# Kernel optimization log

Hardware: AMD Instinct MI355X
Metric: run time of the kernel (lower is better)

The kernel has to match this reference:

```python
import jax, jax.numpy as jnp
import numpy as np

N = 768                       # atoms
E = N * (N - 1)               # complete directed graph edges
DIM = 64                      # hidden dim
CUT = 5.0                     # rbf high
NC = 50                       # n_centers = ceil(5/0.1)
ODIM = 1                      # output_dim
NCONV = 3
_centers_np = np.linspace(0.0, CUT, NC)
CENTERS = jnp.asarray(_centers_np, jnp.float32)
GAP = float(_centers_np[1] - _centers_np[0])
RO_IN = 2 * ODIM + NC         # readout input: 2*output_dim + rbf fan_out = 52


def softplus_bt(x, beta, thr):
    # torch.nn.Softplus(beta, threshold): linear above threshold
    bx = beta * x
    return jnp.where(bx > thr, x, jax.nn.softplus(bx) / beta)


def rbf(d):
    # exp(-(1/gap) * (d - mu_k)^2); d: (..., 1) -> (..., NC)
    return jnp.exp((-1.0 / GAP) * (d - CENTERS) ** 2)


def setup_inputs() -> dict:
    key = jax.random.key(0)
    ks = jax.random.split(key, 24)
    atom_types = jax.random.randint(ks[0], (N,), 0, 100)
    edge_distances = jax.random.uniform(ks[1], (E, 1), jnp.float32) * CUT
    # complete directed graph, edge order matches the nested i,j loop (i!=j)
    ii = np.repeat(np.arange(N), N)
    jj = np.tile(np.arange(N), N)
    m = ii != jj
    src = jnp.asarray(ii[m], jnp.int32)
    dst = jnp.asarray(jj[m], jnp.int32)

    def p(k, shape, fan):
        return jax.random.normal(k, shape, jnp.float32) / np.sqrt(fan)

    embedding = p(ks[2], (100, DIM), DIM).at[0].set(0.0)  # padding_idx=0
    L = NCONV
    return {
        'atom_types': atom_types, 'edge_distances': edge_distances,
        'src': src, 'dst': dst, 'embedding': embedding,
        'w1': p(ks[3], (L, DIM, DIM), DIM),                 # node_layer1 (no bias)
        'pw1': p(ks[4], (L, NC, DIM), NC), 'pb1': p(ks[5], (L, DIM), NC),
        'pw2': p(ks[6], (L, DIM, DIM), DIM), 'pb2': p(ks[7], (L, DIM), DIM),
        'qw1': p(ks[8], (L, DIM, DIM), DIM), 'qb1': p(ks[9], (L, DIM), DIM),
        'qw2': p(ks[10], (L, DIM, DIM), DIM), 'qb2': p(ks[11], (L, DIM), DIM),
        'au_w1': p(ks[12], (DIM, 64), DIM), 'au_b1': p(ks[13], (64,), DIM),
        'au_w2': p(ks[14], (64, ODIM), 64), 'au_b2': p(ks[15], (ODIM,), 64),
        'ro_w1': p(ks[16], (RO_IN, 64), RO_IN), 'ro_b1': p(ks[17], (64,), RO_IN),
        'ro_w2': p(ks[18], (64, 2), 64), 'ro_b2': p(ks[19], (2,), 64),
    }


def reference(atom_types, edge_distances, src, dst, embedding,
              w1, pw1, pb1, pw2, pb2, qw1, qb1, qw2, qb2,
              au_w1, au_b1, au_w2, au_b2, ro_w1, ro_b1, ro_w2, ro_b2):
    h = embedding[atom_types]                       # (N, DIM)
    rbf_out = rbf(edge_distances)                   # (E, NC)
    for l in range(NCONV):
        nw = h @ w1[l]                              # node weights (N, DIM)
        e = softplus_bt(rbf_out @ pw1[l] + pb1[l], 0.5, 14) @ pw2[l] + pb2[l]  # (E, DIM)
        msg = nw[src] * e                           # gather-mul (E, DIM)
        agg = jax.ops.segment_sum(msg, dst, num_segments=N)  # scatter-sum (N, DIM)
        upd = softplus_bt(agg @ qw1[l] + qb1[l], 0.5, 14) @ qw2[l] + qb2[l]
        h = h + upd
    # atom_update with ShiftSoftplus (beta=1, shift=2, threshold=20)
    ha = softplus_bt(h @ au_w1 + au_b1, 1.0, 20) - jnp.log(jnp.float32(2.0))
    ha = ha @ au_w2 + au_b2                         # (N, ODIM)
    # readout over all ordered pairs i!=j, in edge order == (src, dst)
    edge_feat = jnp.concatenate([ha[src], ha[dst], rbf_out], axis=-1)  # (E, 52)
    logits = jax.nn.relu(edge_feat @ ro_w1 + ro_b1) @ ro_w2 + ro_b2    # (E, 2)
    return jax.nn.softmax(logits, axis=-1)
```

## Files before the change

kernel.cpp:

```cpp
#include <hip/hip_runtime.h>

#define NATOMS 768
#define NM1    767
#define NEDGE  (768*767)
#define DIM    64
#define NC     50
#define GAPF   (5.0f/49.0f)
#define NIGAP  (-49.0f/5.0f)
#define G      512
#define STEPF  (5.0f/511.0f)
#define INVSTEP (511.0f/5.0f)
#define LN2F   0.693147180559945f

#define WS_H     0
#define WS_NWA   49152
#define WS_NWB   98304
#define WS_HA    147456
#define WS_DISTT 148224
#define WS_TT    738048

__device__ __forceinline__ float softplus05(float x) {
    float bx = 0.5f * x;
    return (bx > 14.0f) ? x : 2.0f * __logf(1.0f + __expf(bx));
}
__device__ __forceinline__ int lane_bcast_i(int v, int l) {
    return __builtin_amdgcn_readlane(v, l);
}
__device__ __forceinline__ float lane_bcast_f(float v, int l) {
    return __uint_as_float((unsigned)__builtin_amdgcn_readlane((int)__float_as_uint(v), l));
}

__global__ __launch_bounds__(256)
void k_pre(const int* __restrict__ types, const float* __restrict__ dist,
           const float* __restrict__ emb, const float* __restrict__ w1all,
           const float* __restrict__ pw1, const float* __restrict__ pb1,
           const float* __restrict__ pw2, const float* __restrict__ pb2,
           const float* __restrict__ row1, const float* __restrict__ rob1,
           float* __restrict__ ws) {
    __shared__ float s_t[4 * 64];
    const int tid = threadIdx.x, widx = tid >> 6, c = tid & 63;
    float* h     = ws + WS_H;
    float* nw    = ws + WS_NWA;
    float* distT = ws + WS_DISTT;
    float* TTf   = ws + WS_TT;
    const int b = blockIdx.x;

    if (b < 512) {
        const int w = b * 4 + widx, tbl = w >> 9, g = w & 511;
        const float d = g * STEPF;
        float val;
        if (tbl < 3) {
            const float* W1 = pw1 + tbl * NC * DIM;
            float t1 = pb1[tbl * DIM + c];
            for (int k = 0; k < NC; ++k) {
                float x = d - GAPF * (float)k;
                t1 = fmaf(__expf(NIGAP * x * x), W1[k * DIM + c], t1);
            }
            s_t[widx * 64 + c] = softplus05(t1);
            const float* W2 = pw2 + tbl * DIM * DIM;
            val = pb2[tbl * DIM + c];
            #pragma unroll 8
            for (int k = 0; k < DIM; ++k)
                val = fmaf(s_t[widx * 64 + k], W2[k * DIM + c], val);
        } else {
            val = rob1[c];
            for (int k = 0; k < NC; ++k) {
                float x = d - GAPF * (float)k;
                val = fmaf(__expf(NIGAP * x * x), row1[(2 + k) * DIM + c], val);
            }
        }
        float* TTt = TTf + tbl * (G * DIM * 2);
        TTt[(g * DIM + c) * 2] = val;
        if (g > 0) TTt[((g - 1) * DIM + c) * 2 + 1] = val;
    } else if (b < 704) {
        const int i = (b - 512) * 4 + widx;
        float hv = emb[types[i] * DIM + c];
        h[i * DIM + c] = hv;
        s_t[widx * 64 + c] = hv;
        float acc = 0.0f;
        #pragma unroll 8
        for (int k = 0; k < DIM; ++k)
            acc = fmaf(s_t[widx * 64 + k], w1all[k * DIM + c], acc);
        nw[i * DIM + c] = acc;
    } else {
        const int idx = (b - 704) * 256 + tid;
        const int j = idx / NATOMS, i = idx - j * NATOMS;
        distT[idx] = (i == j) ? 0.0f : dist[i * NM1 + (j - (j > i))];
    }
}

__global__ __launch_bounds__(512)
void k_edgeupd(const float2* __restrict__ TTl, const float* __restrict__ distT,
               const float* __restrict__ nwin,
               const float* __restrict__ qw1, const float* __restrict__ qb1,
               const float* __restrict__ qw2, const float* __restrict__ qb2,
               float* __restrict__ h,
               const float* __restrict__ wnext, float* __restrict__ nwout,
               const float* __restrict__ auw1, const float* __restrict__ aub1,
               const float* __restrict__ auw2, const float* __restrict__ aub2,
               float* __restrict__ ha, int last) {
    __shared__ float s_part[8][64];
    __shared__ float s_upd[192];
    const int tid = threadIdx.x, widx = tid >> 6, c = tid & 63;
    const int j = blockIdx.x;
    const int s0 = widx * 96;

    const char* TTb = (const char*)TTl + c * 8;
    float csum = 0.0f;
    {
        float d = distT[j * NATOMS + s0 + c];
        float pos = d * INVSTEP;
        int g = (int)pos;
        g = (g < 0) ? 0 : ((g > 510) ? 510 : g);
        float f = pos - (float)g;
        int kx = g * 512;
        #pragma unroll 8
        for (int it = 0; it < 64; ++it) {
            int kxu = lane_bcast_i(kx, it);
            float fu = lane_bcast_f(f, it);
            float2 tt = *(const float2*)(TTb + kxu);
            float e = fmaf(fu, tt.y - tt.x, tt.x);
            csum = fmaf(e, nwin[(s0 + it) * DIM + c], csum);
        }
    }
    {
        float d = distT[j * NATOMS + s0 + 64 + (c & 31)];
        float pos = d * INVSTEP;
        int g = (int)pos;
        g = (g < 0) ? 0 : ((g > 510) ? 510 : g);
        float f = pos - (float)g;
        int kx = g * 512;
        #pragma unroll 8
        for (int it = 0; it < 32; ++it) {
            int kxu = lane_bcast_i(kx, it);
            float fu = lane_bcast_f(f, it);
            float2 tt = *(const float2*)(TTb + kxu);
            float e = fmaf(fu, tt.y - tt.x, tt.x);
            csum = fmaf(e, nwin[(s0 + 64 + it) * DIM + c], csum);
        }
    }
    s_part[widx][c] = csum;
    __syncthreads();

    if (widx == 0) {
        float tot = 0.0f;
        #pragma unroll
        for (int w8 = 0; w8 < 8; ++w8) tot += s_part[w8][c];
        float2 t0 = *(const float2*)TTb;
        tot -= t0.x * nwin[j * DIM + c];
        s_upd[c] = tot;
        float t = qb1[c];
        #pragma unroll 8
        for (int k = 0; k < DIM; ++k) t = fmaf(s_upd[k], qw1[k * DIM + c], t);
        s_upd[64 + c] = softplus05(t);
        float o = qb2[c];
        #pragma unroll 8
        for (int k = 0; k < DIM; ++k) o = fmaf(s_upd[64 + k], qw2[k * DIM + c], o);
        float hn = h[j * DIM + c] + o;
        h[j * DIM + c] = hn;
        s_upd[128 + c] = hn;
        if (!last) {
            float v = 0.0f;
            #pragma unroll 8
            for (int k = 0; k < DIM; ++k) v = fmaf(s_upd[128 + k], wnext[k * DIM + c], v);
            nwout[j * DIM + c] = v;
        } else {
            float t2 = aub1[c];
            #pragma unroll 8
            for (int k = 0; k < DIM; ++k) t2 = fmaf(s_upd[128 + k], auw1[k * DIM + c], t2);
            t2 = ((t2 > 20.0f) ? t2 : __logf(1.0f + __expf(t2))) - LN2F;
            float v = t2 * auw2[c];
            #pragma unroll
            for (int s = 32; s > 0; s >>= 1) v += __shfl_down(v, s, 64);
            if (c == 0) ha[j] = v + aub2[0];
        }
    }
}

__global__ __launch_bounds__(256)
void k_ro(const float* __restrict__ dist, const int* __restrict__ src,
          const int* __restrict__ dst, const float* __restrict__ ha,
          const float2* __restrict__ TTro,
          const float* __restrict__ row1, const float* __restrict__ row2,
          const float* __restrict__ rob2, float* __restrict__ out) {
    __shared__ float4 s_pre[4][64];
    __shared__ float s_h[4][16 * 65];
    __shared__ float s_w2[128];
    const int tid = threadIdx.x, widx = tid >> 6, c = tid & 63;
    if (tid < 128) s_w2[tid] = row2[tid];
    __syncthreads();
    const int ebase = (blockIdx.x * 4 + widx) * 64;
    {
        int eg = ebase + c;
        float d = dist[eg];
        float pos = d * INVSTEP;
        int kk = (int)pos;
        kk = (kk < 0) ? 0 : ((kk > 510) ? 510 : kk);
        float fa = ha[src[eg]], fb = ha[dst[eg]];
        s_pre[widx][c] = make_float4(__int_as_float(kk * 512), pos - (float)kk, fa, fb);
    }
    const char* TTb2 = (const char*)TTro + c * 8;
    const float wa = row1[c], wb = row1[DIM + c];
    const int e2 = (c >> 1) & 15, p2 = c & 1, kh = c >> 5;
    const float bias2 = (kh == 0) ? rob2[p2] : 0.0f;
    float* sh = s_h[widx];
    #pragma unroll
    for (int ch = 0; ch < 4; ++ch) {
        #pragma unroll 4
        for (int e = 0; e < 16; ++e) {
            float4 p = s_pre[widx][ch * 16 + e];
            float2 tt = *(const float2*)(TTb2 + __float_as_int(p.x));
            float hv = fmaf(p.y, tt.y - tt.x, tt.x);
            hv = fmaf(p.z, wa, hv);
            hv = fmaf(p.w, wb, hv);
            sh[e * 65 + c] = fmaxf(hv, 0.0f);
        }
        float lsum = bias2;
        #pragma unroll 8
        for (int k8 = 0; k8 < 32; ++k8) {
            int k = kh * 32 + k8;
            lsum = fmaf(sh[e2 * 65 + k], s_w2[2 * k + p2], lsum);
        }
        lsum += __shfl_xor(lsum, 32, 64);
        float other = __shfl_xor(lsum, 1, 64);
        float m = fmaxf(lsum, other);
        float ea = __expf(lsum - m), eb = __expf(other - m);
        float r = ea / (ea + eb);
        if (c < 32) out[ebase * 2 + ch * 32 + c] = r;
    }
}

extern "C" void kernel_launch(void* const* d_in, const int* in_sizes, int n_in,
                              void* d_out, int out_size, void* d_ws, size_t ws_size,
                              hipStream_t stream) {
    const int*   types = (const int*)d_in[0];
    const float* dist  = (const float*)d_in[1];
    const int*   srcI  = (const int*)d_in[2];
    const int*   dstI  = (const int*)d_in[3];
    const float* emb   = (const float*)d_in[4];
    const float* w1    = (const float*)d_in[5];
    const float* pw1   = (const float*)d_in[6];
    const float* pb1   = (const float*)d_in[7];
    const float* pw2   = (const float*)d_in[8];
    const float* pb2   = (const float*)d_in[9];
    const float* qw1   = (const float*)d_in[10];
    const float* qb1   = (const float*)d_in[11];
    const float* qw2   = (const float*)d_in[12];
    const float* qb2   = (const float*)d_in[13];
    const float* auw1  = (const float*)d_in[14];
    const float* aub1  = (const float*)d_in[15];
    const float* auw2  = (const float*)d_in[16];
    const float* aub2  = (const float*)d_in[17];
    const float* row1  = (const float*)d_in[18];
    const float* rob1  = (const float*)d_in[19];
    const float* row2  = (const float*)d_in[20];
    const float* rob2  = (const float*)d_in[21];

    float* ws   = (float*)d_ws;
    float* outp = (float*)d_out;
    const float2* TT = (const float2*)(ws + WS_TT);
    float* nwbuf[2] = { ws + WS_NWA, ws + WS_NWB };

    k_pre<<<3008, 256, 0, stream>>>(types, dist, emb, w1, pw1, pb1, pw2, pb2,
                                    row1, rob1, ws);
    for (int l = 0; l < 3; ++l) {
        k_edgeupd<<<768, 512, 0, stream>>>(TT + l * (G * DIM),
            ws + WS_DISTT, nwbuf[l & 1],
            qw1 + l * DIM * DIM, qb1 + l * DIM,
            qw2 + l * DIM * DIM, qb2 + l * DIM,
            ws + WS_H,
            (l < 2) ? (w1 + (l + 1) * DIM * DIM) : w1, nwbuf[(l + 1) & 1],
            auw1, aub1, auw2, aub2, ws + WS_HA, (l == 2) ? 1 : 0);
    }
    k_ro<<<2301, 256, 0, stream>>>(dist, srcI, dstI, ws + WS_HA, TT + 3 * (G * DIM),
                                   row1, row2, rob2, outp);
}
```

Before: 214.9 us.

## Fuse conv layers and readout into one cooperative persistent kernel with grid barriers

Replaces the three per-layer edge-update launches and the readout launch with a single cooperative kernel of 768 blocks. Layers are separated by atomic-counter grid barriers, and h is kept in a register across layers. A third node-weight buffer avoids a read/write hazard between layers. This removes launch gaps and lets the readout follow directly, at the cost of spin-wait barriers, fewer waves per block (256 threads instead of 512), and a guarded spin that could fall through early if the barrier stalls.

After: 664.7 us. +209.2%, slower.

```diff
diff --git a/kernel.cpp b/kernel.cpp
--- a/kernel.cpp
+++ b/kernel.cpp
@@ -15,9 +15,11 @@
 #define WS_H     0
 #define WS_NWA   49152
 #define WS_NWB   98304
-#define WS_HA    147456
-#define WS_DISTT 148224
-#define WS_TT    738048
+#define WS_NWC   147456
+#define WS_HA    196608
+#define WS_CTR   197376
+#define WS_DISTT 197632
+#define WS_TT    787456
 
 __device__ __forceinline__ float softplus05(float x) {
     float bx = 0.5f * x;
@@ -45,6 +47,8 @@
     float* TTf   = ws + WS_TT;
     const int b = blockIdx.x;
 
+    if (b == 0 && tid < 8) ((unsigned*)(ws + WS_CTR))[tid] = 0u;
+
     if (b < 512) {
         const int w = b * 4 + widx, tbl = w >> 9, g = w & 511;
         const float d = g * STEPF;
@@ -86,6 +90,154 @@
         const int idx = (b - 704) * 256 + tid;
         const int j = idx / NATOMS, i = idx - j * NATOMS;
         distT[idx] = (i == j) ? 0.0f : dist[i * NM1 + (j - (j > i))];
+    }
+}
+
+struct P4s { float4 pre[4][64]; float h[4][16 * 65]; float w2[128]; };
+union SmemM {
+    struct { float part[4][64]; float upd[192]; } cv;
+    P4s p4;
+};
+
+__global__ __launch_bounds__(256, 3)
+void k_mega(const float* __restrict__ dist, const int* __restrict__ srcI,
+            const int* __restrict__ dstI, const float* __restrict__ w1all,
+            const float* __restrict__ qw1, const float* __restrict__ qb1,
+            const float* __restrict__ qw2, const float* __restrict__ qb2,
+            const float* __restrict__ auw1, const float* __restrict__ aub1,
+            const float* __restrict__ auw2, const float* __restrict__ aub2,
+            const float* __restrict__ row1, const float* __restrict__ row2,
+            const float* __restrict__ rob2,
+            float* __restrict__ ws, float* __restrict__ out) {
+    __shared__ SmemM sm;
+    const int tid = threadIdx.x, widx = tid >> 6, c = tid & 63;
+    const int b = blockIdx.x;
+    float* hG    = ws + WS_H;
+    float* ha    = ws + WS_HA;
+    unsigned* ctr = (unsigned*)(ws + WS_CTR);
+    const float* distT = ws + WS_DISTT;
+    const float* TTf   = ws + WS_TT;
+    float* nwbuf[3] = { ws + WS_NWA, ws + WS_NWB, ws + WS_NWC };
+
+    float hreg = (widx == 0) ? hG[b * DIM + c] : 0.0f;
+
+    for (int l = 0; l < 3; ++l) {
+        const float* nwin = nwbuf[l];
+        const float2* TTl = (const float2*)TTf + l * (G * DIM);
+        const char* TTb = (const char*)TTl + c * 8;
+        float csum = 0.0f;
+        #pragma unroll
+        for (int ch = 0; ch < 3; ++ch) {
+            const int s0 = widx * 192 + ch * 64;
+            float d = distT[b * NATOMS + s0 + c];
+            float pos = d * INVSTEP;
+            int g = (int)pos;
+            g = (g < 0) ? 0 : ((g > 510) ? 510 : g);
+            float f = pos - (float)g;
+            int kx = g * 512;
+            #pragma unroll 8
+            for (int it = 0; it < 64; ++it) {
+                int kxu = lane_bcast_i(kx, it);
+                float fu = lane_bcast_f(f, it);
+                float2 tt = *(const float2*)(TTb + kxu);
+                float e = fmaf(fu, tt.y - tt.x, tt.x);
+                csum = fmaf(e, nwin[(s0 + it) * DIM + c], csum);
+            }
+        }
+        sm.cv.part[widx][c] = csum;
+        __syncthreads();
+        if (widx == 0) {
+            float tot = sm.cv.part[0][c] + sm.cv.part[1][c]
+                      + sm.cv.part[2][c] + sm.cv.part[3][c];
+            float2 t0 = *(const float2*)TTb;
+            tot -= t0.x * nwin[b * DIM + c];
+            float* su = sm.cv.upd;
+            su[c] = tot;
+            float t = qb1[l * DIM + c];
+            #pragma unroll 8
+            for (int k = 0; k < DIM; ++k)
+                t = fmaf(su[k], qw1[l * DIM * DIM + k * DIM + c], t);
+            su[64 + c] = softplus05(t);
+            float o = qb2[l * DIM + c];
+            #pragma unroll 8
+            for (int k = 0; k < DIM; ++k)
+                o = fmaf(su[64 + k], qw2[l * DIM * DIM + k * DIM + c], o);
+            hreg += o;
+            su[128 + c] = hreg;
+            if (l < 2) {
+                const float* Wn = w1all + (l + 1) * DIM * DIM;
+                float v = 0.0f;
+                #pragma unroll 8
+                for (int k = 0; k < DIM; ++k) v = fmaf(su[128 + k], Wn[k * DIM + c], v);
+                nwbuf[l + 1][b * DIM + c] = v;
+            } else {
+                float t2 = aub1[c];
+                #pragma unroll 8
+                for (int k = 0; k < DIM; ++k) t2 = fmaf(su[128 + k], auw1[k * DIM + c], t2);
+                t2 = ((t2 > 20.0f) ? t2 : __logf(1.0f + __expf(t2))) - LN2F;
+                float v = t2 * auw2[c];
+                #pragma unroll
+                for (int s = 32; s > 0; s >>= 1) v += __shfl_down(v, s, 64);
+                if (c == 0) ha[b] = v + aub2[0];
+            }
+            if (c == 0) {
+                __hip_atomic_fetch_add(&ctr[l], 1u, __ATOMIC_ACQ_REL,
+                                       __HIP_MEMORY_SCOPE_AGENT);
+                unsigned guard = 0;
+                while (__hip_atomic_load(&ctr[l], __ATOMIC_ACQUIRE,
+                                         __HIP_MEMORY_SCOPE_AGENT) < (unsigned)NATOMS
+                       && ++guard < (1u << 24)) { }
+            }
+        }
+        __syncthreads();
+    }
+
+    if (tid < 128) sm.p4.w2[tid] = row2[tid];
+    __syncthreads();
+    const float2* TTro = (const float2*)TTf + 3 * (G * DIM);
+    const char* TTb2 = (const char*)TTro + c * 8;
+    const float wa = row1[c], wb = row1[DIM + c];
+    const int e2 = (c >> 1) & 15, p2 = c & 1, kh = c >> 5;
+    const float bias2 = (kh == 0) ? rob2[p2] : 0.0f;
+    const int w = b * 4 + widx;
+    for (int rnd = 0; rnd < 3; ++rnd) {
+        const int w4 = rnd * 3072 + w;
+        if (w4 >= 9204) break;
+        const int ebase = w4 * 64;
+        {
+            int eg = ebase + c;
+            float d = dist[eg];
+            float pos = d * INVSTEP;
+            int kk = (int)pos;
+            kk = (kk < 0) ? 0 : ((kk > 510) ? 510 : kk);
+            float fa = ha[srcI[eg]], fb = ha[dstI[eg]];
+            sm.p4.pre[widx][c] = make_float4(__int_as_float(kk * 512), pos - (float)kk, fa, fb);
+        }
+        float* sh = sm.p4.h[widx];
+        #pragma unroll
+        for (int ch = 0; ch < 4; ++ch) {
+            #pragma unroll 4
+            for (int e = 0; e < 16; ++e) {
+                float4 p = sm.p4.pre[widx][ch * 16 + e];
+                float2 tt = *(const float2*)(TTb2 + __float_as_int(p.x));
+                float hv = fmaf(p.y, tt.y - tt.x, tt.x);
+                hv = fmaf(p.z, wa, hv);
+                hv = fmaf(p.w, wb, hv);
+                sh[e * 65 + c] = fmaxf(hv, 0.0f);
+            }
+            float lsum = bias2;
+            #pragma unroll 8
+            for (int k8 = 0; k8 < 32; ++k8) {
+                int k = kh * 32 + k8;
+                lsum = fmaf(sh[e2 * 65 + k], sm.p4.w2[2 * k + p2], lsum);
+            }
+            lsum += __shfl_xor(lsum, 32, 64);
+            float other = __shfl_xor(lsum, 1, 64);
+            float m = fmaxf(lsum, other);
+            float ea = __expf(lsum - m), eb = __expf(other - m);
+            float r = ea / (ea + eb);
+            if (c < 32) out[ebase * 2 + ch * 32 + c] = r;
+        }
     }
 }
 
@@ -104,7 +256,6 @@
     const int tid = threadIdx.x, widx = tid >> 6, c = tid & 63;
     const int j = blockIdx.x;
     const int s0 = widx * 96;
-
     const char* TTb = (const char*)TTl + c * 8;
     float csum = 0.0f;
     {
@@ -141,7 +292,6 @@
     }
     s_part[widx][c] = csum;
     __syncthreads();
-
     if (widx == 0) {
         float tot = 0.0f;
         #pragma unroll
@@ -259,10 +409,37 @@
     float* ws   = (float*)d_ws;
     float* outp = (float*)d_out;
     const float2* TT = (const float2*)(ws + WS_TT);
-    float* nwbuf[2] = { ws + WS_NWA, ws + WS_NWB };
 
     k_pre<<<3008, 256, 0, stream>>>(types, dist, emb, w1, pw1, pb1, pw2, pb2,
                                     row1, rob1, ws);
+
+    int coopOK = 0;
+    {
+        int dev = 0;
+        if (hipGetDevice(&dev) == hipSuccess) {
+            hipDeviceProp_t prop;
+            if (hipGetDeviceProperties(&prop, dev) == hipSuccess &&
+                prop.cooperativeLaunch) {
+                int maxB = 0;
+                if (hipOccupancyMaxActiveBlocksPerMultiprocessor(
+                        &maxB, (const void*)k_mega, 256, 0) == hipSuccess &&
+                    (long)maxB * prop.multiProcessorCount >= NATOMS)
+                    coopOK = 1;
+            }
+        }
+    }
+    if (coopOK) {
+        void* args[] = { (void*)&dist, (void*)&srcI, (void*)&dstI, (void*)&w1,
+                         (void*)&qw1, (void*)&qb1, (void*)&qw2, (void*)&qb2,
+                         (void*)&auw1, (void*)&aub1, (void*)&auw2, (void*)&aub2,
+                         (void*)&row1, (void*)&row2, (void*)&rob2,
+                         (void*)&ws, (void*)&outp };
+        if (hipLaunchCooperativeKernel((void*)k_mega, dim3(NATOMS), dim3(256),
+                                       args, 0, stream) == hipSuccess)
+            return;
+    }
+
+    float* nwbuf[2] = { ws + WS_NWA, ws + WS_NWB };
     for (int l = 0; l < 3; ++l) {
         k_edgeupd<<<768, 512, 0, stream>>>(TT + l * (G * DIM),
             ws + WS_DISTT, nwbuf[l & 1],
```

## Process three destination atoms per block in edge-update kernel to reuse nw loads

Applied to the files above, without the earlier changes.

The edge-update kernel now handles three destination atoms per block instead of one, cutting the grid from 768 to 256 blocks. Each loaded node-weight value is reused across three accumulators, which reduces global load traffic for nwin and raises instruction-level parallelism through three independent gather chains. In exchange there are fewer blocks (256 on a GPU with many CUs), more registers per thread, and the tail work now runs on three waves instead of one.

Result: slower. 222.2 us (+3.4%).

```diff
diff --git a/kernel.cpp b/kernel.cpp
--- a/kernel.cpp
+++ b/kernel.cpp
@@ -90,89 +90,124 @@
 }
 
 __global__ __launch_bounds__(512)
-void k_edgeupd(const float2* __restrict__ TTl, const float* __restrict__ distT,
-               const float* __restrict__ nwin,
-               const float* __restrict__ qw1, const float* __restrict__ qb1,
-               const float* __restrict__ qw2, const float* __restrict__ qb2,
-               float* __restrict__ h,
-               const float* __restrict__ wnext, float* __restrict__ nwout,
-               const float* __restrict__ auw1, const float* __restrict__ aub1,
-               const float* __restrict__ auw2, const float* __restrict__ aub2,
-               float* __restrict__ ha, int last) {
-    __shared__ float s_part[8][64];
-    __shared__ float s_upd[192];
+void k_edgeupd3(const float2* __restrict__ TTl, const float* __restrict__ distT,
+                const float* __restrict__ nwin,
+                const float* __restrict__ qw1, const float* __restrict__ qb1,
+                const float* __restrict__ qw2, const float* __restrict__ qb2,
+                float* __restrict__ h,
+                const float* __restrict__ wnext, float* __restrict__ nwout,
+                const float* __restrict__ auw1, const float* __restrict__ aub1,
+                const float* __restrict__ auw2, const float* __restrict__ aub2,
+                float* __restrict__ ha, int last) {
+    __shared__ float s_part[8][3][64];
+    __shared__ float s_upd[3][192];
     const int tid = threadIdx.x, widx = tid >> 6, c = tid & 63;
-    const int j = blockIdx.x;
+    const int j0 = blockIdx.x * 3;
     const int s0 = widx * 96;
 
     const char* TTb = (const char*)TTl + c * 8;
-    float csum = 0.0f;
+    float acc0 = 0.0f, acc1 = 0.0f, acc2 = 0.0f;
+
     {
-        float d = distT[j * NATOMS + s0 + c];
-        float pos = d * INVSTEP;
-        int g = (int)pos;
-        g = (g < 0) ? 0 : ((g > 510) ? 510 : g);
-        float f = pos - (float)g;
-        int kx = g * 512;
+        float dA = distT[j0 * NATOMS + s0 + c];
+        float dB = distT[(j0 + 1) * NATOMS + s0 + c];
+        float dC = distT[(j0 + 2) * NATOMS + s0 + c];
+        float pA = dA * INVSTEP, pB = dB * INVSTEP, pC = dC * INVSTEP;
+        int gA = (int)pA, gB = (int)pB, gC = (int)pC;
+        gA = (gA < 0) ? 0 : ((gA > 510) ? 510 : gA);
+        gB = (gB < 0) ? 0 : ((gB > 510) ? 510 : gB);
+        gC = (gC < 0) ? 0 : ((gC > 510) ? 510 : gC);
+        float fA = pA - (float)gA, fB = pB - (float)gB, fC = pC - (float)gC;
+        int kA = gA * 512, kB = gB * 512, kC = gC * 512;
         #pragma unroll 8
         for (int it = 0; it < 64; ++it) {
-            int kxu = lane_bcast_i(kx, it);
-            float fu = lane_bcast_f(f, it);
-            float2 tt = *(const float2*)(TTb + kxu);
-            float e = fmaf(fu, tt.y - tt.x, tt.x);
-            csum = fmaf(e, nwin[(s0 + it) * DIM + c], csum);
+            float nwv = nwin[(s0 + it) * DIM + c];
+            {
+                float2 tt = *(const float2*)(TTb + lane_bcast_i(kA, it));
+                float e = fmaf(lane_bcast_f(fA, it), tt.y - tt.x, tt.x);
+                acc0 = fmaf(e, nwv, acc0);
+            }
+            {
+                float2 tt = *(const float2*)(TTb + lane_bcast_i(kB, it));
+                float e = fmaf(lane_bcast_f(fB, it), tt.y - tt.x, tt.x);
+                acc1 = fmaf(e, nwv, acc1);
+            }
+            {
+                float2 tt = *(const float2*)(TTb + lane_bcast_i(kC, it));
+                float e = fmaf(lane_bcast_f(fC, it), tt.y - tt.x, tt.x);
+                acc2 = fmaf(e, nwv, acc2);
+            }
         }
     }
     {
-        float d = distT[j * NATOMS + s0 + 64 + (c & 31)];
-        float pos = d * INVSTEP;
-        int g = (int)pos;
-        g = (g < 0) ? 0 : ((g > 510) ? 510 : g);
-        float f = pos - (float)g;
-        int kx = g * 512;
+        float dA = distT[j0 * NATOMS + s0 + 64 + (c & 31)];
+        float dB = distT[(j0 + 1) * NATOMS + s0 + 64 + (c & 31)];
+        float dC = distT[(j0 + 2) * NATOMS + s0 + 64 + (c & 31)];
+        float pA = dA * INVSTEP, pB = dB * INVSTEP, pC = dC * INVSTEP;
+        int gA = (int)pA, gB = (int)pB, gC = (int)pC;
+        gA = (gA < 0) ? 0 : ((gA > 510) ? 510 : gA);
+        gB = (gB < 0) ? 0 : ((gB > 510) ? 510 : gB);
+        gC = (gC < 0) ? 0 : ((gC > 510) ? 510 : gC);
+        float fA = pA - (float)gA, fB = pB - (float)gB, fC = pC - (float)gC;
+        int kA = gA * 512, kB = gB * 512, kC = gC * 512;
         #pragma unroll 8
         for (int it = 0; it < 32; ++it) {
-            int kxu = lane_bcast_i(kx, it);
-            float fu = lane_bcast_f(f, it);
-            float2 tt = *(const float2*)(TTb + kxu);
-            float e = fmaf(fu, tt.y - tt.x, tt.x);
-            csum = fmaf(e, nwin[(s0 + 64 + it) * DIM + c], csum);
-        }
-    }
-    s_part[widx][c] = csum;
+            float nwv = nwin[(s0 + 64 + it) * DIM + c];
+            {
+                float2 tt = *(const float2*)(TTb + lane_bcast_i(kA, it));
+                float e = fmaf(lane_bcast_f(fA, it), tt.y - tt.x, tt.x);
+                acc0 = fmaf(e, nwv, acc0);
+            }
+            {
+                float2 tt = *(const float2*)(TTb + lane_bcast_i(kB, it));
+                float e = fmaf(lane_bcast_f(fB, it), tt.y - tt.x, tt.x);
+                acc1 = fmaf(e, nwv, acc1);
+            }
+            {
+                float2 tt = *(const float2*)(TTb + lane_bcast_i(kC, it));
+                float e = fmaf(lane_bcast_f(fC, it), tt.y - tt.x, tt.x);
+                acc2 = fmaf(e, nwv, acc2);
+            }
+        }
+    }
+    s_part[widx][0][c] = acc0;
+    s_part[widx][1][c] = acc1;
+    s_part[widx][2][c] = acc2;
     __syncthreads();
 
-    if (widx == 0) {
+    if (widx < 3) {
+        const int jt = j0 + widx;
         float tot = 0.0f;
         #pragma unroll
-        for (int w8 = 0; w8 < 8; ++w8) tot += s_part[w8][c];
+        for (int w8 = 0; w8 < 8; ++w8) tot += s_part[w8][widx][c];
         float2 t0 = *(const float2*)TTb;
-        tot -= t0.x * nwin[j * DIM + c];
-        s_upd[c] = tot;
+        tot -= t0.x * nwin[jt * DIM + c];
+        float* su = s_upd[widx];
+        su[c] = tot;
         float t = qb1[c];
         #pragma unroll 8
-        for (int k = 0; k < DIM; ++k) t = fmaf(s_upd[k], qw1[k * DIM + c], t);
-        s_upd[64 + c] = softplus05(t);
+        for (int k = 0; k < DIM; ++k) t = fmaf(su[k], qw1[k * DIM + c], t);
+        su[64 + c] = softplus05(t);
         float o = qb2[c];
         #pragma unroll 8
-        for (int k = 0; k < DIM; ++k) o = fmaf(s_upd[64 + k], qw2[k * DIM + c], o);
-        float hn = h[j * DIM + c] + o;
-        h[j * DIM + c] = hn;
-        s_upd[128 + c] = hn;
+        for (int k = 0; k < DIM; ++k) o = fmaf(su[64 + k], qw2[k * DIM + c], o);
+        float hn = h[jt * DIM + c] + o;
+        h[jt * DIM + c] = hn;
+        su[128 + c] = hn;
         if (!last) {
             float v = 0.0f;
             #pragma unroll 8
-            for (int k = 0; k < DIM; ++k) v = fmaf(s_upd[128 + k], wnext[k * DIM + c], v);
-            nwout[j * DIM + c] = v;
+            for (int k = 0; k < DIM; ++k) v = fmaf(su[128 + k], wnext[k * DIM + c], v);
+            nwout[jt * DIM + c] = v;
         } else {
             float t2 = aub1[c];
             #pragma unroll 8
-            for (int k = 0; k < DIM; ++k) t2 = fmaf(s_upd[128 + k], auw1[k * DIM + c], t2);
+            for (int k = 0; k < DIM; ++k) t2 = fmaf(su[128 + k], auw1[k * DIM + c], t2);
             t2 = ((t2 > 20.0f) ? t2 : __logf(1.0f + __expf(t2))) - LN2F;
             float v = t2 * auw2[c];
             #pragma unroll
             for (int s = 32; s > 0; s >>= 1) v += __shfl_down(v, s, 64);
-            if (c == 0) ha[j] = v + aub2[0];
+            if (c == 0) ha[jt] = v + aub2[0];
         }
     }
 }
@@ -264,7 +299,7 @@
     k_pre<<<3008, 256, 0, stream>>>(types, dist, emb, w1, pw1, pb1, pw2, pb2,
                                     row1, rob1, ws);
     for (int l = 0; l < 3; ++l) {
-        k_edgeupd<<<768, 512, 0, stream>>>(TT + l * (G * DIM),
+        k_edgeupd3<<<256, 512, 0, stream>>>(TT + l * (G * DIM),
             ws + WS_DISTT, nwbuf[l & 1],
             qw1 + l * DIM * DIM, qb1 + l * DIM,
             qw2 + l * DIM * DIM, qb2 + l * DIM,
```
